# Kernel optimization log

Measured on AMD Instinct MI355X. Metric: run time of the kernel, lower is better.

## Reference

```python
import jax, jax.numpy as jnp
import numpy as np

BN_EPS = 1e-5


def _feat_proj(x, w1, w2, gamma, beta):
    # FactorLinear2D: (N,L,C) @ w2^T -> (N,L,K); weighted sum over L with w1^T -> (N,K)
    h = jnp.einsum('nlc,kc->nlk', x, w2)
    h = jnp.einsum('nlk,kl->nk', h, w1)
    # BatchNorm1d, training mode (biased batch stats), affine
    mu = h.mean(axis=0)
    var = h.var(axis=0)
    return gamma * (h - mu) * jax.lax.rsqrt(var + BN_EPS) + beta


def setup_inputs() -> dict:
    key = jax.random.key(0)
    ks = jax.random.split(key, 16)
    N, G, H, P, K = 64, 8, 1024, 2048, 39548
    s = 0.02
    return {
        'x0': jax.random.normal(ks[0], (N, 257, 1024), jnp.float32),
        'x1': jax.random.normal(ks[1], (N, 197, 768), jnp.float32),
        'w1_0': s * jax.random.normal(ks[2], (H, 257), jnp.float32),
        'w2_0': s * jax.random.normal(ks[3], (H, 1024), jnp.float32),
        'gamma0': jnp.ones((H,), jnp.float32),
        'beta0': jnp.zeros((H,), jnp.float32),
        'w1_1': s * jax.random.normal(ks[4], (H, 197), jnp.float32),
        'w2_1': s * jax.random.normal(ks[5], (H, 768), jnp.float32),
        'gamma1': jnp.ones((H,), jnp.float32),
        'beta1': jnp.zeros((H,), jnp.float32),
        'shared_w': s * jax.random.normal(ks[6], (P, H), jnp.float32),
        'fc_w': s * jax.random.normal(ks[7], (G * P, H), jnp.float32),
        'fc_b': s * jax.random.normal(ks[8], (G * P,), jnp.float32),
        'embed_w': s * jax.random.normal(ks[9], (K, P), jnp.float32),
        'embed_b': s * jax.random.normal(ks[10], (K,), jnp.float32),
        'indices': jax.random.randint(ks[11], (64,), 0, G, jnp.int64),
    }


def reference(x0, x1, w1_0, w2_0, gamma0, beta0, w1_1, w2_1, gamma1, beta1,
              shared_w, fc_w, fc_b, embed_w, embed_b, indices):
    G = 8
    h0 = _feat_proj(x0, w1_0, w2_0, gamma0, beta0)  # (N,H)
    h1 = _feat_proj(x1, w1_1, w2_1, gamma1, beta1)  # (N,H)
    latent = 0.5 * (h0 + h1)                        # mean over feature list
    # group prediction: embed(shared_proj(latent))
    group_pred = (latent @ shared_w.T) @ embed_w.T + embed_b  # (N,K)
    # subject-specific GroupLinear: gather per-sample weight slice, then reduced matmul
    P = fc_w.shape[0] // G
    w_sel = fc_w.reshape(G, P, -1)[indices]   # (N,P,H)
    b_sel = fc_b.reshape(G, P)[indices]       # (N,P)
    subj = jnp.einsum('nh,nph->np', latent, w_sel) + b_sel
    subj_res = subj @ embed_w.T + embed_b
    return group_pred + subj_res
```

## Files before the change

### kernel.cpp

```cpp
#include <hip/hip_runtime.h>
#include <hip/hip_bf16.h>


typedef __attribute__((ext_vector_type(4))) float f32x4;
typedef __attribute__((ext_vector_type(8))) short bf16x8;

__device__ __forceinline__ short f2bf(float v) {
  __hip_bfloat16 h = __float2bfloat16(v);
  union { __hip_bfloat16 b; short s; } u; u.b = h; return u.s;
}

__device__ __forceinline__ void gload16(const short* g, short* l) {
  __builtin_amdgcn_global_load_lds(
      (const __attribute__((address_space(1))) void*)g,
      (__attribute__((address_space(3))) void*)l, 16, 0, 0);
}

__device__ __forceinline__ void gload16f(const float* g, float* l) {
  __builtin_amdgcn_global_load_lds(
      (const __attribute__((address_space(1))) void*)g,
      (__attribute__((address_space(3))) void*)l, 16, 0, 0);
}

__device__ __forceinline__ void cvt8(const float* __restrict__ in,
                                     short* __restrict__ out, size_t i) {
  const float4* p = reinterpret_cast<const float4*>(in) + 2 * i;
  float4 a = p[0], b = p[1];
  bf16x8 o;
  o[0] = f2bf(a.x); o[1] = f2bf(a.y); o[2] = f2bf(a.z); o[3] = f2bf(a.w);
  o[4] = f2bf(b.x); o[5] = f2bf(b.y); o[6] = f2bf(b.z); o[7] = f2bf(b.w);
  *reinterpret_cast<bf16x8*>(out + 8 * i) = o;
}

__global__ __launch_bounds__(256) void prep(
    const float* __restrict__ x0, const float* __restrict__ x1,
    const float* __restrict__ w20, const float* __restrict__ w21,
    const float* __restrict__ w10, const float* __restrict__ w11,
    short* __restrict__ x0b, short* __restrict__ x1b,
    short* __restrict__ w20b, short* __restrict__ w21b,
    float* __restrict__ w1t0, float* __restrict__ w1t1,
    float* __restrict__ zz)
{
  __shared__ float tile[32][33];
  if (blockIdx.x >= 13968) {
    int b = blockIdx.x - 13968;
    const float* src; float* dst; int Lw;
    if (b < 288) { src = w10; dst = w1t0; Lw = 257; }
    else         { b -= 288; src = w11; dst = w1t1; Lw = 197; }
    int kt = b & 31, lt = b >> 5;
    int c = threadIdx.x & 31, r8 = threadIdx.x >> 5;
#pragma unroll
    for (int i = 0; i < 4; ++i) {
      int a = r8 + 8 * i;
      int l = lt * 32 + c;
      tile[a][c] = (l < Lw) ? src[(size_t)(kt * 32 + a) * Lw + l] : 0.f;
    }
    __syncthreads();
#pragma unroll
    for (int i = 0; i < 4; ++i) {
      int bl = r8 + 8 * i;
      int l = lt * 32 + bl;
      if (l < Lw) dst[(size_t)l * 1024 + kt * 32 + c] = tile[c][bl];
    }
    return;
  }
  size_t i = (size_t)blockIdx.x * 256 + threadIdx.x;
  const size_t C0 = 2105344;
  const size_t C1 = C0 + 8192;
  const size_t C2 = C1 + 1210368;
  const size_t C3 = C2 + 6144;
  const size_t C4 = C3 + 131072;
  const size_t C5 = C4 + 98304;
  if (i < C0) { cvt8(x0, x0b, i); return; }
  if (i < C1) {
    bf16x8 zv = {};
    *reinterpret_cast<bf16x8*>(x0b + (size_t)16448 * 1024 + 8 * (i - C0)) = zv;
    return;
  }
  if (i < C2) { cvt8(x1, x1b, i - C1); return; }
  if (i < C3) {
    bf16x8 zv = {};
    *reinterpret_cast<bf16x8*>(x1b + (size_t)12608 * 768 + 8 * (i - C2)) = zv;
    return;
  }
  if (i < C4) { cvt8(w20, w20b, i - C3); return; }
  if (i < C5) { cvt8(w21, w21b, i - C4); return; }
  f32x4 z4 = {};
  f32x4* zp = reinterpret_cast<f32x4*>(zz) + 2 * (i - C5);
  zp[0] = z4; zp[1] = z4;
}

template<int L>
__device__ __forceinline__ void fused_body(
    const short* __restrict__ Ab, const short* __restrict__ Bb,
    const float* __restrict__ w1t, float* __restrict__ z,
    int Mpad, int M, int K, int orig, short* As, short* Bs, float* zacc, int tid)
{
  const int lane = tid & 63;
  const int wave = tid >> 6;
  const int wm = wave >> 1, wn = wave & 1;
  const int tile_m = (orig >> 3) * 256;
  const int tile_n = (orig & 7) * 128;
  const int rl = lane & 15;
  const int lh = lane >> 4;

  zacc[tid] = 0.f;

  f32x4 acc[4][4] = {};
  const int nt = K >> 5;

  auto stage = [&](short* dA, short* dB, int k0) {
#pragma unroll
    for (int c = 0; c < 2; ++c) {
      int o = (c * 512 + tid) * 16;
      int r = o >> 6;
      int sc = ((o >> 4) & 3) ^ ((r >> 1) & 3);
      int gr = tile_m + r; if (gr >= Mpad) gr = Mpad - 1;
      gload16(Ab + (size_t)gr * K + k0 + sc * 8, (short*)((char*)dA + o));
    }
    {
      int o = tid * 16;
      int r = o >> 6;
      int sc = ((o >> 4) & 3) ^ ((r >> 1) & 3);
      gload16(Bb + (size_t)(tile_n + r) * K + k0 + sc * 8, (short*)((char*)dB + o));
    }
  };

  stage(As, Bs, 0);
  int cur = 0;
  for (int t = 0; t < nt; ++t) {
    if (t + 1 < nt) {
      stage(As + (cur ^ 1) * 8192, Bs + (cur ^ 1) * 4096, (t + 1) * 32);
      asm volatile("s_waitcnt vmcnt(3)" ::: "memory");
    } else {
      asm volatile("s_waitcnt vmcnt(0)" ::: "memory");
    }
    __builtin_amdgcn_s_barrier();
    __builtin_amdgcn_sched_barrier(0);
    const char* pa = (const char*)(As + cur * 8192);
    const char* pb = (const char*)(Bs + cur * 4096);
    bf16x8 af[4], bfr[4];
#pragma unroll
    for (int mi = 0; mi < 4; ++mi) {
      int r = wm * 64 + mi * 16 + rl;
      int j = lh ^ ((r >> 1) & 3);
      af[mi] = *reinterpret_cast<const bf16x8*>(pa + r * 64 + j * 16);
    }
#pragma unroll
    for (int ni = 0; ni < 4; ++ni) {
      int r = wn * 64 + ni * 16 + rl;
      int j = lh ^ ((r >> 1) & 3);
      bfr[ni] = *reinterpret_cast<const bf16x8*>(pb + r * 64 + j * 16);
    }
    __builtin_amdgcn_s_setprio(1);
#pragma unroll
    for (int mi = 0; mi < 4; ++mi)
#pragma unroll
      for (int ni = 0; ni < 4; ++ni)
        acc[mi][ni] = __builtin_amdgcn_mfma_f32_16x16x32_bf16(af[mi], bfr[ni], acc[mi][ni], 0, 0, 0);
    __builtin_amdgcn_s_setprio(0);
    __builtin_amdgcn_sched_barrier(0);
    __builtin_amdgcn_s_barrier();
    __builtin_amdgcn_sched_barrier(0);
    cur ^= 1;
  }

  const int nbase = tile_m / L;
#pragma unroll
  for (int ni = 0; ni < 4; ++ni) {
    int colL = wn * 64 + ni * 16 + rl;
    int col = tile_n + colL;
    float zac = 0.f;
    int curdn = -1;
#pragma unroll
    for (int mi = 0; mi < 4; ++mi) {
#pragma unroll
      for (int j = 0; j < 4; ++j) {
        int row = tile_m + wm * 64 + mi * 16 + lh * 4 + j;
        if (row < M) {
          int n = row / L, l = row - n * L;
          float v = acc[mi][ni][j] * w1t[(size_t)l * 1024 + col];
          int dn = n - nbase;
          if (dn != curdn) {
            if (curdn >= 0) atomicAdd(&zacc[curdn * 128 + colL], zac);
            curdn = dn; zac = 0.f;
          }
          zac += v;
        }
      }
    }
    if (curdn >= 0) atomicAdd(&zacc[curdn * 128 + colL], zac);
  }
  __syncthreads();
  {
    int dn = tid >> 7, c = tid & 127;
    int mtop = tile_m + 255; if (mtop > M - 1) mtop = M - 1;
    int nhi = mtop / L;
    int n = nbase + dn;
    if (n <= nhi)
      atomicAdd(z + (size_t)n * 1024 + tile_n + c, zacc[tid]);
  }
}

__global__ __launch_bounds__(512) void gemm_fused_dual(
    const short* __restrict__ x0b, const short* __restrict__ w20b,
    const float* __restrict__ w1t0, float* __restrict__ z0,
    const short* __restrict__ x1b, const short* __restrict__ w21b,
    const float* __restrict__ w1t1, float* __restrict__ z1)
{
  __shared__ short As[2 * 8192];
  __shared__ short Bs[2 * 4096];
  __shared__ float zacc[512];
  const int flat = blockIdx.x;
  const int tid = threadIdx.x;
  if (flat < 520) {
    const int orig = (flat & 7) * 65 + (flat >> 3);
    fused_body<257>(x0b, w20b, w1t0, z0, 16512, 16448, 1024, orig, As, Bs, zacc, tid);
  } else {
    const int f = flat - 520;
    const int orig = (f & 7) * 50 + (f >> 3);
    fused_body<197>(x1b, w21b, w1t1, z1, 12672, 12608, 768, orig, As, Bs, zacc, tid);
  }
}

__global__ void bn_latent(const float* __restrict__ z0, const float* __restrict__ z1,
                          const float* __restrict__ g0, const float* __restrict__ b0,
                          const float* __restrict__ g1, const float* __restrict__ b1,
                          float* __restrict__ lat)
{
  int k = blockIdx.x * blockDim.x + threadIdx.x;
  if (k >= 1024) return;
  float s0 = 0.f, q0 = 0.f, s1 = 0.f, q1 = 0.f;
  for (int n = 0; n < 64; ++n) {
    float v = z0[n * 1024 + k]; s0 += v; q0 += v * v;
    float w = z1[n * 1024 + k]; s1 += w; q1 += w * w;
  }
  float mu0 = s0 * (1.f / 64.f), var0 = q0 * (1.f / 64.f) - mu0 * mu0;
  float mu1 = s1 * (1.f / 64.f), var1 = q1 * (1.f / 64.f) - mu1 * mu1;
  float sc0 = g0[k] * rsqrtf(var0 + 1e-5f);
  float sc1 = g1[k] * rsqrtf(var1 + 1e-5f);
  float be0 = b0[k], be1 = b1[k];
  for (int n = 0; n < 64; ++n) {
    float v = sc0 * (z0[n * 1024 + k] - mu0) + be0
            + sc1 * (z1[n * 1024 + k] - mu1) + be1;
    lat[n * 1024 + k] = 0.5f * v;
  }
}

__global__ __launch_bounds__(512) void s_combine(
    const float* __restrict__ lat, const float* __restrict__ sw,
    const float* __restrict__ fw, const float* __restrict__ fb,
    const int* __restrict__ idx, short* __restrict__ sb)
{
  __shared__ int nlist[64];
  __shared__ int ncnt;
  const int g  = blockIdx.x >> 5;
  const int pc = blockIdx.x & 31;
  const int tid = threadIdx.x;
  const int lane = tid & 63;
  const int wave = tid >> 6;

  if (wave == 0) {
    int match = (idx[lane] == g) ? 1 : 0;
    unsigned long long m = __ballot(match);
    if (match) {
      int pos = __popcll(m & ((1ull << lane) - 1ull));
      nlist[pos] = lane;
    }
    if (lane == 0) ncnt = __popcll(m);
  }
  __syncthreads();
  const int cnt = ncnt;
  if (cnt == 0) return;

  for (int c0 = 0; c0 < cnt; c0 += 8) {
    const int nc = (cnt - c0 < 8) ? (cnt - c0) : 8;
    f32x4 latr[8][4];
#pragma unroll
    for (int j2 = 0; j2 < 8; ++j2)
      if (j2 < nc) {
        const f32x4* lp = reinterpret_cast<const f32x4*>(lat + (size_t)nlist[c0 + j2] * 1024);
#pragma unroll
        for (int q = 0; q < 4; ++q) latr[j2][q] = lp[q * 64 + lane];
      }
#pragma unroll 2
    for (int pi = 0; pi < 8; ++pi) {
      int p = pc * 64 + wave * 8 + pi;
      const f32x4* fp = reinterpret_cast<const f32x4*>(fw + ((size_t)g * 2048 + p) * 1024);
      const f32x4* sp = reinterpret_cast<const f32x4*>(sw + (size_t)p * 1024);
      f32x4 row[4];
#pragma unroll
      for (int q = 0; q < 4; ++q) row[q] = fp[q * 64 + lane] + sp[q * 64 + lane];
      float bias = fb[(size_t)g * 2048 + p];
#pragma unroll
      for (int j2 = 0; j2 < 8; ++j2)
        if (j2 < nc) {
          float d = 0.f;
#pragma unroll
          for (int q = 0; q < 4; ++q) {
            d = fmaf(row[q][0], latr[j2][q][0], d);
            d = fmaf(row[q][1], latr[j2][q][1], d);
            d = fmaf(row[q][2], latr[j2][q][2], d);
            d = fmaf(row[q][3], latr[j2][q][3], d);
          }
          d += __shfl_xor(d, 32); d += __shfl_xor(d, 16);
          d += __shfl_xor(d, 8);  d += __shfl_xor(d, 4);
          d += __shfl_xor(d, 2);  d += __shfl_xor(d, 1);
          if (lane == 0)
            sb[(size_t)nlist[c0 + j2] * 2048 + p] = f2bf(d + bias);
        }
    }
  }
}

__global__ __launch_bounds__(256) void gemm_embed(
    const short* __restrict__ sb, const float* __restrict__ E,
    const float* __restrict__ eb, float* __restrict__ out)
{
  __shared__ short As[2 * 64 * 64];
  __shared__ float Bs[2 * 64 * 64];
  const int tid  = threadIdx.x;
  const int lane = tid & 63;
  const int wave = tid >> 6;
  const int rl = lane & 15;
  const int lh = lane >> 4;
  const int tile_n = blockIdx.x * 64;

  auto stage = [&](int buf, int k0) {
#pragma unroll
    for (int c = 0; c < 2; ++c) {
      int o = (c * 256 + tid) * 16;
      int r = o >> 7;
      int cc = ((o >> 4) & 7) ^ (r & 7);
      gload16(sb + (size_t)r * 2048 + k0 + cc * 8,
              (short*)((char*)(As + buf * 4096) + o));
    }
#pragma unroll
    for (int c = 0; c < 4; ++c) {
      int o = (c * 256 + tid) * 16;
      int r = o >> 8;
      int cc = ((o >> 4) & 15) ^ (r & 15);
      int gr = tile_n + r; if (gr > 39547) gr = 39547;
      gload16f(E + (size_t)gr * 2048 + k0 + cc * 4,
               (float*)((char*)(Bs + buf * 4096) + o));
    }
  };

  f32x4 acc[4] = {};
  stage(0, 0);
  int cur = 0;
  for (int t = 0; t < 32; ++t) {
    if (t < 31) {
      stage(cur ^ 1, (t + 1) * 64);
      asm volatile("s_waitcnt vmcnt(6)" ::: "memory");
    } else {
      asm volatile("s_waitcnt vmcnt(0)" ::: "memory");
    }
    __builtin_amdgcn_s_barrier();
    __builtin_amdgcn_sched_barrier(0);
    const char* pa = (const char*)(As + cur * 4096);
    const char* pb = (const char*)(Bs + cur * 4096);
#pragma unroll
    for (int ks = 0; ks < 2; ++ks) {
      int br = wave * 16 + rl;
      int c0 = ks * 8 + lh * 2;
      f32x4 u = *reinterpret_cast<const f32x4*>(pb + br * 256 + ((c0 ^ (br & 15)) * 16));
      f32x4 v = *reinterpret_cast<const f32x4*>(pb + br * 256 + (((c0 + 1) ^ (br & 15)) * 16));
      bf16x8 bf;
      bf[0] = f2bf(u[0]); bf[1] = f2bf(u[1]); bf[2] = f2bf(u[2]); bf[3] = f2bf(u[3]);
      bf[4] = f2bf(v[0]); bf[5] = f2bf(v[1]); bf[6] = f2bf(v[2]); bf[7] = f2bf(v[3]);
#pragma unroll
      for (int mi = 0; mi < 4; ++mi) {
        int ar = mi * 16 + rl;
        int ac = (ks * 4 + lh) ^ (ar & 7);
        bf16x8 af = *reinterpret_cast<const bf16x8*>(pa + ar * 128 + ac * 16);
        acc[mi] = __builtin_amdgcn_mfma_f32_16x16x32_bf16(af, bf, acc[mi], 0, 0, 0);
      }
    }
    __builtin_amdgcn_sched_barrier(0);
    __builtin_amdgcn_s_barrier();
    __builtin_amdgcn_sched_barrier(0);
    cur ^= 1;
  }

  int col = tile_n + wave * 16 + rl;
  if (col < 39548) {
    float bi = 2.f * eb[col];
#pragma unroll
    for (int mi = 0; mi < 4; ++mi)
#pragma unroll
      for (int j = 0; j < 4; ++j) {
        int n = mi * 16 + lh * 4 + j;
        out[(size_t)n * 39548 + col] = acc[mi][j] + bi;
      }
  }
}

extern "C" void kernel_launch(void* const* d_in, const int* in_sizes, int n_in,
                              void* d_out, int out_size, void* d_ws, size_t ws_size,
                              hipStream_t stream)
{
  const float* x0       = (const float*)d_in[0];
  const float* x1       = (const float*)d_in[1];
  const float* w1_0     = (const float*)d_in[2];
  const float* w2_0     = (const float*)d_in[3];
  const float* gamma0   = (const float*)d_in[4];
  const float* beta0    = (const float*)d_in[5];
  const float* w1_1     = (const float*)d_in[6];
  const float* w2_1     = (const float*)d_in[7];
  const float* gamma1   = (const float*)d_in[8];
  const float* beta1    = (const float*)d_in[9];
  const float* shared_w = (const float*)d_in[10];
  const float* fc_w     = (const float*)d_in[11];
  const float* fc_b     = (const float*)d_in[12];
  const float* embed_w  = (const float*)d_in[13];
  const float* embed_b  = (const float*)d_in[14];
  const int*   indices  = (const int*)d_in[15];
  float* out = (float*)d_out;

  short* x0b  = (short*)d_ws;
  short* x1b  = x0b + (size_t)16512 * 1024;
  short* w20b = x1b + (size_t)12672 * 768;
  short* w21b = w20b + (size_t)1024 * 1024;
  float* w1t0 = (float*)(w21b + (size_t)1024 * 768);
  float* w1t1 = w1t0 + (size_t)257 * 1024;
  float* z0   = w1t1 + (size_t)197 * 1024;
  float* z1   = z0 + 64 * 1024;
  float* lat  = z1 + 64 * 1024;
  short* sb   = (short*)(lat + 64 * 1024);

  prep<<<14480, 256, 0, stream>>>(x0, x1, w2_0, w2_1, w1_0, w1_1,
                                  x0b, x1b, w20b, w21b, w1t0, w1t1, z0);

  gemm_fused_dual<<<920, 512, 0, stream>>>(x0b, w20b, w1t0, z0,
                                           x1b, w21b, w1t1, z1);

  bn_latent<<<16, 64, 0, stream>>>(z0, z1, gamma0, beta0, gamma1, beta1, lat);
  s_combine<<<256, 512, 0, stream>>>(lat, shared_w, fc_w, fc_b, indices, sb);

  gemm_embed<<<618, 256, 0, stream>>>(sb, embed_w, embed_b, out);
}
```

Baseline: 241.3 us.

## Split embed GEMM over K into two halves with a separate reduction kernel

The final embedding GEMM now runs as a 2-way split-K over the 2048-long reduction, with the K tile shrunk from 64 to 32. This doubles the block count and halves shared memory per block, so more blocks can be resident while streaming the large fp32 embedding matrix. Each half writes fp32 partials into the reused workspace, and a new elementwise kernel sums them and adds twice the bias. The cost is an extra launch, extra partial-sum traffic, and twice as many barriers per unit of K.

```diff
diff --git a/kernel.cpp b/kernel.cpp
--- a/kernel.cpp
+++ b/kernel.cpp
@@ -315,67 +315,64 @@
 
 __global__ __launch_bounds__(256) void gemm_embed(
     const short* __restrict__ sb, const float* __restrict__ E,
-    const float* __restrict__ eb, float* __restrict__ out)
-{
-  __shared__ short As[2 * 64 * 64];
-  __shared__ float Bs[2 * 64 * 64];
+    float* __restrict__ part)
+{
+  __shared__ short As[2 * 64 * 32];
+  __shared__ float Bs[2 * 64 * 32];
   const int tid  = threadIdx.x;
   const int lane = tid & 63;
   const int wave = tid >> 6;
   const int rl = lane & 15;
   const int lh = lane >> 4;
   const int tile_n = blockIdx.x * 64;
+  const int kbeg = blockIdx.y * 1024;
 
   auto stage = [&](int buf, int k0) {
+    {
+      int o = tid * 16;
+      int r = o >> 6;
+      int cc = ((o >> 4) & 3) ^ ((r >> 1) & 3);
+      gload16(sb + (size_t)r * 2048 + k0 + cc * 8,
+              (short*)((char*)(As + buf * 2048) + o));
+    }
 #pragma unroll
     for (int c = 0; c < 2; ++c) {
       int o = (c * 256 + tid) * 16;
       int r = o >> 7;
       int cc = ((o >> 4) & 7) ^ (r & 7);
-      gload16(sb + (size_t)r * 2048 + k0 + cc * 8,
-              (short*)((char*)(As + buf * 4096) + o));
-    }
-#pragma unroll
-    for (int c = 0; c < 4; ++c) {
-      int o = (c * 256 + tid) * 16;
-      int r = o >> 8;
-      int cc = ((o >> 4) & 15) ^ (r & 15);
       int gr = tile_n + r; if (gr > 39547) gr = 39547;
       gload16f(E + (size_t)gr * 2048 + k0 + cc * 4,
-               (float*)((char*)(Bs + buf * 4096) + o));
+               (float*)((char*)(Bs + buf * 2048) + o));
     }
   };
 
   f32x4 acc[4] = {};
-  stage(0, 0);
+  stage(0, kbeg);
   int cur = 0;
   for (int t = 0; t < 32; ++t) {
     if (t < 31) {
-      stage(cur ^ 1, (t + 1) * 64);
-      asm volatile("s_waitcnt vmcnt(6)" ::: "memory");
+      stage(cur ^ 1, kbeg + (t + 1) * 32);
+      asm volatile("s_waitcnt vmcnt(3)" ::: "memory");
     } else {
       asm volatile("s_waitcnt vmcnt(0)" ::: "memory");
     }
     __builtin_amdgcn_s_barrier();
     __builtin_amdgcn_sched_barrier(0);
-    const char* pa = (const char*)(As + cur * 4096);
-    const char* pb = (const char*)(Bs + cur * 4096);
-#pragma unroll
-    for (int ks = 0; ks < 2; ++ks) {
-      int br = wave * 16 + rl;
-      int c0 = ks * 8 + lh * 2;
-      f32x4 u = *reinterpret_cast<const f32x4*>(pb + br * 256 + ((c0 ^ (br & 15)) * 16));
-      f32x4 v = *reinterpret_cast<const f32x4*>(pb + br * 256 + (((c0 + 1) ^ (br & 15)) * 16));
-      bf16x8 bf;
-      bf[0] = f2bf(u[0]); bf[1] = f2bf(u[1]); bf[2] = f2bf(u[2]); bf[3] = f2bf(u[3]);
-      bf[4] = f2bf(v[0]); bf[5] = f2bf(v[1]); bf[6] = f2bf(v[2]); bf[7] = f2bf(v[3]);
-#pragma unroll
-      for (int mi = 0; mi < 4; ++mi) {
-        int ar = mi * 16 + rl;
-        int ac = (ks * 4 + lh) ^ (ar & 7);
-        bf16x8 af = *reinterpret_cast<const bf16x8*>(pa + ar * 128 + ac * 16);
-        acc[mi] = __builtin_amdgcn_mfma_f32_16x16x32_bf16(af, bf, acc[mi], 0, 0, 0);
-      }
+    const char* pa = (const char*)(As + cur * 2048);
+    const char* pb = (const char*)(Bs + cur * 2048);
+    int br = wave * 16 + rl;
+    int c0 = lh * 2;
+    f32x4 u = *reinterpret_cast<const f32x4*>(pb + br * 128 + ((c0 ^ (br & 7)) * 16));
+    f32x4 v = *reinterpret_cast<const f32x4*>(pb + br * 128 + (((c0 + 1) ^ (br & 7)) * 16));
+    bf16x8 bf;
+    bf[0] = f2bf(u[0]); bf[1] = f2bf(u[1]); bf[2] = f2bf(u[2]); bf[3] = f2bf(u[3]);
+    bf[4] = f2bf(v[0]); bf[5] = f2bf(v[1]); bf[6] = f2bf(v[2]); bf[7] = f2bf(v[3]);
+#pragma unroll
+    for (int mi = 0; mi < 4; ++mi) {
+      int ar = mi * 16 + rl;
+      int ac = lh ^ ((ar >> 1) & 3);
+      bf16x8 af = *reinterpret_cast<const bf16x8*>(pa + ar * 64 + ac * 16);
+      acc[mi] = __builtin_amdgcn_mfma_f32_16x16x32_bf16(af, bf, acc[mi], 0, 0, 0);
     }
     __builtin_amdgcn_sched_barrier(0);
     __builtin_amdgcn_s_barrier();
@@ -385,15 +382,35 @@
 
   int col = tile_n + wave * 16 + rl;
   if (col < 39548) {
-    float bi = 2.f * eb[col];
+    float* Cp = part + (size_t)blockIdx.y * 64 * 39548;
 #pragma unroll
     for (int mi = 0; mi < 4; ++mi)
 #pragma unroll
       for (int j = 0; j < 4; ++j) {
         int n = mi * 16 + lh * 4 + j;
-        out[(size_t)n * 39548 + col] = acc[mi][j] + bi;
+        Cp[(size_t)n * 39548 + col] = acc[mi][j];
       }
   }
+}
+
+__global__ __launch_bounds__(256) void reduce_out(
+    const float* __restrict__ part, const float* __restrict__ eb,
+    float* __restrict__ out)
+{
+  const int NT = 39548;
+  const size_t S = (size_t)64 * NT / 4;
+  size_t i = (size_t)blockIdx.x * 256 + threadIdx.x;
+  if (i >= S) return;
+  const f32x4* p = reinterpret_cast<const f32x4*>(part);
+  f32x4 a = p[i] + p[i + S];
+  int col = (int)(i % (NT / 4)) * 4;
+  f32x4 b = *reinterpret_cast<const f32x4*>(eb + col);
+  f32x4 r;
+  r[0] = a[0] + 2.f * b[0];
+  r[1] = a[1] + 2.f * b[1];
+  r[2] = a[2] + 2.f * b[2];
+  r[3] = a[3] + 2.f * b[3];
+  reinterpret_cast<f32x4*>(out)[i] = r;
 }
 
 extern "C" void kernel_launch(void* const* d_in, const int* in_sizes, int n_in,
@@ -428,6 +445,7 @@
   float* z1   = z0 + 64 * 1024;
   float* lat  = z1 + 64 * 1024;
   short* sb   = (short*)(lat + 64 * 1024);
+  float* part = (float*)d_ws;
 
   prep<<<14480, 256, 0, stream>>>(x0, x1, w2_0, w2_1, w1_0, w1_1,
                                   x0b, x1b, w20b, w21b, w1t0, w1t1, z0);
@@ -438,5 +456,6 @@
   bn_latent<<<16, 64, 0, stream>>>(z0, z1, gamma0, beta0, gamma1, beta1, lat);
   s_combine<<<256, 512, 0, stream>>>(lat, shared_w, fc_w, fc_b, indices, sb);
 
-  gemm_embed<<<618, 256, 0, stream>>>(sb, embed_w, embed_b, out);
-}
+  gemm_embed<<<dim3(618, 2), 256, 0, stream>>>(sb, embed_w, part);
+  reduce_out<<<2472, 256, 0, stream>>>(part, embed_b, out);
+}
```

Result: slower. 263.3 us (+9.1%).

## Retile fused GEMM to 128x128 blocks with single-buffered 64-wide K steps

Applied to the files above, without the earlier changes.

The fused projection GEMM moves from 256x128 tiles with 512 threads and a double-buffered 32-wide K pipeline to 128x128 tiles with 256 threads. It now uses a single LDS buffer, 64-wide K steps and an 8-way XOR swizzle, and roughly doubles the grid. The aim is more blocks in flight and less LDS per block, so occupancy can hide load latency in place of explicit prefetching. In exchange it drops the load/compute overlap, adds two full barriers per K step, and loses the setprio hints. The row clamping to Mpad is removed, so the last tiles rely on the padded rows of the bf16 buffers.

```diff
diff --git a/kernel.cpp b/kernel.cpp
--- a/kernel.cpp
+++ b/kernel.cpp
@@ -94,75 +94,61 @@
 __device__ __forceinline__ void fused_body(
     const short* __restrict__ Ab, const short* __restrict__ Bb,
     const float* __restrict__ w1t, float* __restrict__ z,
-    int Mpad, int M, int K, int orig, short* As, short* Bs, float* zacc, int tid)
+    int M, int K, int orig, short* As, short* Bs, float* zacc, int tid)
 {
   const int lane = tid & 63;
   const int wave = tid >> 6;
   const int wm = wave >> 1, wn = wave & 1;
-  const int tile_m = (orig >> 3) * 256;
+  const int tile_m = (orig >> 3) * 128;
   const int tile_n = (orig & 7) * 128;
   const int rl = lane & 15;
   const int lh = lane >> 4;
 
-  zacc[tid] = 0.f;
+  if (tid < 256) zacc[tid] = 0.f;
 
   f32x4 acc[4][4] = {};
-  const int nt = K >> 5;
-
-  auto stage = [&](short* dA, short* dB, int k0) {
-#pragma unroll
-    for (int c = 0; c < 2; ++c) {
-      int o = (c * 512 + tid) * 16;
-      int r = o >> 6;
-      int sc = ((o >> 4) & 3) ^ ((r >> 1) & 3);
-      int gr = tile_m + r; if (gr >= Mpad) gr = Mpad - 1;
-      gload16(Ab + (size_t)gr * K + k0 + sc * 8, (short*)((char*)dA + o));
-    }
-    {
-      int o = tid * 16;
-      int r = o >> 6;
-      int sc = ((o >> 4) & 3) ^ ((r >> 1) & 3);
-      gload16(Bb + (size_t)(tile_n + r) * K + k0 + sc * 8, (short*)((char*)dB + o));
-    }
-  };
-
-  stage(As, Bs, 0);
-  int cur = 0;
+  const int nt = K >> 6;
+
   for (int t = 0; t < nt; ++t) {
-    if (t + 1 < nt) {
-      stage(As + (cur ^ 1) * 8192, Bs + (cur ^ 1) * 4096, (t + 1) * 32);
-      asm volatile("s_waitcnt vmcnt(3)" ::: "memory");
-    } else {
-      asm volatile("s_waitcnt vmcnt(0)" ::: "memory");
-    }
-    __builtin_amdgcn_s_barrier();
-    __builtin_amdgcn_sched_barrier(0);
-    const char* pa = (const char*)(As + cur * 8192);
-    const char* pb = (const char*)(Bs + cur * 4096);
-    bf16x8 af[4], bfr[4];
-#pragma unroll
-    for (int mi = 0; mi < 4; ++mi) {
-      int r = wm * 64 + mi * 16 + rl;
-      int j = lh ^ ((r >> 1) & 3);
-      af[mi] = *reinterpret_cast<const bf16x8*>(pa + r * 64 + j * 16);
-    }
-#pragma unroll
-    for (int ni = 0; ni < 4; ++ni) {
-      int r = wn * 64 + ni * 16 + rl;
-      int j = lh ^ ((r >> 1) & 3);
-      bfr[ni] = *reinterpret_cast<const bf16x8*>(pb + r * 64 + j * 16);
-    }
-    __builtin_amdgcn_s_setprio(1);
-#pragma unroll
-    for (int mi = 0; mi < 4; ++mi)
-#pragma unroll
-      for (int ni = 0; ni < 4; ++ni)
-        acc[mi][ni] = __builtin_amdgcn_mfma_f32_16x16x32_bf16(af[mi], bfr[ni], acc[mi][ni], 0, 0, 0);
-    __builtin_amdgcn_s_setprio(0);
-    __builtin_amdgcn_sched_barrier(0);
-    __builtin_amdgcn_s_barrier();
-    __builtin_amdgcn_sched_barrier(0);
-    cur ^= 1;
+    const int k0 = t * 64;
+    __syncthreads();
+#pragma unroll
+    for (int c = 0; c < 4; ++c) {
+      int o = (c * 256 + tid) * 16;
+      int r = o >> 7;
+      int cc = ((o >> 4) & 7) ^ (r & 7);
+      gload16(Ab + (size_t)(tile_m + r) * K + k0 + cc * 8, (short*)((char*)As + o));
+    }
+#pragma unroll
+    for (int c = 0; c < 4; ++c) {
+      int o = (c * 256 + tid) * 16;
+      int r = o >> 7;
+      int cc = ((o >> 4) & 7) ^ (r & 7);
+      gload16(Bb + (size_t)(tile_n + r) * K + k0 + cc * 8, (short*)((char*)Bs + o));
+    }
+    __syncthreads();
+
+#pragma unroll
+    for (int ks = 0; ks < 2; ++ks) {
+      bf16x8 af[4], bfr[4];
+#pragma unroll
+      for (int mi = 0; mi < 4; ++mi) {
+        int r = wm * 64 + mi * 16 + rl;
+        int j = (ks * 4 + lh) ^ (r & 7);
+        af[mi] = *reinterpret_cast<const bf16x8*>((const char*)As + r * 128 + j * 16);
+      }
+#pragma unroll
+      for (int ni = 0; ni < 4; ++ni) {
+        int r = wn * 64 + ni * 16 + rl;
+        int j = (ks * 4 + lh) ^ (r & 7);
+        bfr[ni] = *reinterpret_cast<const bf16x8*>((const char*)Bs + r * 128 + j * 16);
+      }
+#pragma unroll
+      for (int mi = 0; mi < 4; ++mi)
+#pragma unroll
+        for (int ni = 0; ni < 4; ++ni)
+          acc[mi][ni] = __builtin_amdgcn_mfma_f32_16x16x32_bf16(af[mi], bfr[ni], acc[mi][ni], 0, 0, 0);
+    }
   }
 
   const int nbase = tile_m / L;
@@ -194,7 +180,7 @@
   __syncthreads();
   {
     int dn = tid >> 7, c = tid & 127;
-    int mtop = tile_m + 255; if (mtop > M - 1) mtop = M - 1;
+    int mtop = tile_m + 127; if (mtop > M - 1) mtop = M - 1;
     int nhi = mtop / L;
     int n = nbase + dn;
     if (n <= nhi)
@@ -202,24 +188,24 @@
   }
 }
 
-__global__ __launch_bounds__(512) void gemm_fused_dual(
+__global__ __launch_bounds__(256) void gemm_fused_dual(
     const short* __restrict__ x0b, const short* __restrict__ w20b,
     const float* __restrict__ w1t0, float* __restrict__ z0,
     const short* __restrict__ x1b, const short* __restrict__ w21b,
     const float* __restrict__ w1t1, float* __restrict__ z1)
 {
-  __shared__ short As[2 * 8192];
-  __shared__ short Bs[2 * 4096];
-  __shared__ float zacc[512];
+  __shared__ short As[128 * 64];
+  __shared__ short Bs[128 * 64];
+  __shared__ float zacc[256];
   const int flat = blockIdx.x;
   const int tid = threadIdx.x;
-  if (flat < 520) {
-    const int orig = (flat & 7) * 65 + (flat >> 3);
-    fused_body<257>(x0b, w20b, w1t0, z0, 16512, 16448, 1024, orig, As, Bs, zacc, tid);
+  if (flat < 1032) {
+    const int orig = (flat & 7) * 129 + (flat >> 3);
+    fused_body<257>(x0b, w20b, w1t0, z0, 16448, 1024, orig, As, Bs, zacc, tid);
   } else {
-    const int f = flat - 520;
-    const int orig = (f & 7) * 50 + (f >> 3);
-    fused_body<197>(x1b, w21b, w1t1, z1, 12672, 12608, 768, orig, As, Bs, zacc, tid);
+    const int f = flat - 1032;
+    const int orig = (f & 7) * 99 + (f >> 3);
+    fused_body<197>(x1b, w21b, w1t1, z1, 12608, 768, orig, As, Bs, zacc, tid);
   }
 }
 
@@ -432,8 +418,8 @@
   prep<<<14480, 256, 0, stream>>>(x0, x1, w2_0, w2_1, w1_0, w1_1,
                                   x0b, x1b, w20b, w21b, w1t0, w1t1, z0);
 
-  gemm_fused_dual<<<920, 512, 0, stream>>>(x0b, w20b, w1t0, z0,
-                                           x1b, w21b, w1t1, z1);
+  gemm_fused_dual<<<1824, 256, 0, stream>>>(x0b, w20b, w1t0, z0,
+                                            x1b, w21b, w1t1, z1);
 
   bn_latent<<<16, 64, 0, stream>>>(z0, z1, gamma0, beta0, gamma1, beta1, lat);
   s_combine<<<256, 512, 0, stream>>>(lat, shared_w, fc_w, fc_b, indices, sb);
```

Result: slower. 268.7 us (+11.4%).
